# Optimization experiments

Hardware: AMD Instinct MI355X
Metric: run time of the kernel (lower is better)

## Reference

```python
import jax, jax.numpy as jnp
import numpy as np

EPS = 1e-5

def _dwconv1d(x, w):
    # x: [B,C,L], w: [C,k] depthwise kernel, same padding, no bias
    k = w.shape[1]
    return jax.lax.conv_general_dilated(
        x, w[:, None, :], window_strides=(1,), padding=[(k // 2, k // 2)],
        dimension_numbers=('NCH', 'OIH', 'NCH'), feature_group_count=x.shape[1])

def _bn1d(x, gamma, beta, mean, var):
    # eval-mode BatchNorm over channel dim of [B,C,L]
    scale = gamma / jnp.sqrt(var + EPS)
    return (x - mean[:, None]) * scale[:, None] + beta[:, None]

def _strip_pool(x, w3, w7, gamma, beta, mean, var):
    # mean of [identity, dwconv_k3, dwconv_k7] then BN
    out = (x + _dwconv1d(x, w3) + _dwconv1d(x, w7)) / 3.0
    return _bn1d(out, gamma, beta, mean, var)

def _hswish(x):
    return x * jnp.clip(x + 3.0, 0.0, 6.0) / 6.0

def setup_inputs() -> dict:
    key = jax.random.key(0)
    ks = jax.random.split(key, 8)
    B, C, H, W = 32, 256, 64, 64   # C = 2*inp
    MIP = 8                        # max(8, 128//32)
    O = 256                        # 2*oup
    f32 = jnp.float32
    x = jax.random.normal(ks[0], (B, C, H, W), f32)
    def bn_params(k, n):
        k1, k2 = jax.random.split(k)
        return (1.0 + 0.1 * jax.random.normal(k1, (n,), f32),      # gamma
                0.1 * jax.random.normal(k2, (n,), f32),            # beta
                jnp.zeros((n,), f32),                              # running_mean
                jnp.ones((n,), f32))                               # running_var
    sph_g, sph_b, sph_m, sph_v = bn_params(ks[1], C)
    spw_g, spw_b, spw_m, spw_v = bn_params(ks[2], C)
    bn1_g, bn1_b, bn1_m, bn1_v = bn_params(ks[3], MIP)
    s = 0.1
    return {
        'x': x,
        'sph_w3': s * jax.random.normal(ks[4], (C, 3), f32),
        'sph_w7': s * jax.random.normal(ks[4], (C, 7), f32),
        'sph_gamma': sph_g, 'sph_beta': sph_b, 'sph_mean': sph_m, 'sph_var': sph_v,
        'spw_w3': s * jax.random.normal(ks[5], (C, 3), f32),
        'spw_w7': s * jax.random.normal(ks[5], (C, 7), f32),
        'spw_gamma': spw_g, 'spw_beta': spw_b, 'spw_mean': spw_m, 'spw_var': spw_v,
        'conv1_w': s * jax.random.normal(ks[6], (MIP, C), f32),
        'bn1_gamma': bn1_g, 'bn1_beta': bn1_b, 'bn1_mean': bn1_m, 'bn1_var': bn1_v,
        'convh_w': s * jax.random.normal(ks[7], (O, MIP), f32),
        'convw_w': s * jax.random.normal(ks[7], (O, MIP), f32),
    }

def reference(x, sph_w3, sph_w7, sph_gamma, sph_beta, sph_mean, sph_var,
              spw_w3, spw_w7, spw_gamma, spw_beta, spw_mean, spw_var,
              conv1_w, bn1_gamma, bn1_beta, bn1_mean, bn1_var,
              convh_w, convw_w):
    B, C, H, W = x.shape
    # coordinate pooling -> strips [B,C,H] and [B,C,W]
    x_h = jnp.mean(x, axis=3)
    x_w = jnp.mean(x, axis=2)
    # multi-scale strip pooling
    x_h = _strip_pool(x_h, sph_w3, sph_w7, sph_gamma, sph_beta, sph_mean, sph_var)
    x_w = _strip_pool(x_w, spw_w3, spw_w7, spw_gamma, spw_beta, spw_mean, spw_var)
    # shared 1x1 conv + BN + h_swish on concatenated strip [B,C,H+W]
    y = jnp.concatenate([x_h, x_w], axis=2)
    y = jnp.einsum('mc,bcl->bml', conv1_w, y)
    y = _bn1d(y, bn1_gamma, bn1_beta, bn1_mean, bn1_var)
    y = _hswish(y)
    y_h, y_w = y[:, :, :H], y[:, :, H:]
    # per-direction gates [B,O,H] / [B,O,W]
    a_h = jax.nn.sigmoid(jnp.einsum('om,bmh->boh', convh_w, y_h))
    a_w = jax.nn.sigmoid(jnp.einsum('om,bmw->bow', convw_w, y_w))
    return x * a_h[:, :, :, None] * a_w[:, :, None, :]
```

## Files before the change

kernel.cpp:

```cpp
#include <hip/hip_runtime.h>
#include <math.h>

#define EPSF 1e-5f

__global__ __launch_bounds__(256) void k1_pool_strip(
    const float* __restrict__ x,
    const float* __restrict__ sph_w3, const float* __restrict__ sph_w7,
    const float* __restrict__ sph_g,  const float* __restrict__ sph_b,
    const float* __restrict__ sph_m,  const float* __restrict__ sph_v,
    const float* __restrict__ spw_w3, const float* __restrict__ spw_w7,
    const float* __restrict__ spw_g,  const float* __restrict__ spw_b,
    const float* __restrict__ spw_m,  const float* __restrict__ spw_v,
    float* __restrict__ sp)
{
    __shared__ __align__(16) float tile[64][68];
    __shared__ float mh[64];
    __shared__ float mw[64];

    const int plane = blockIdx.x;
    const int c = plane & 255;
    const float* xp = x + (size_t)plane * 4096;
    const int t = threadIdx.x;
    const int r = t >> 2, q = t & 3;

    const float4* src = (const float4*)(xp + r * 64 + q * 16);
    float4* dst = (float4*)&tile[r][q * 16];
    dst[0] = src[0]; dst[1] = src[1]; dst[2] = src[2]; dst[3] = src[3];
    __syncthreads();

    if (t < 64) {
        float s = 0.f;
        for (int rr = 0; rr < 64; ++rr) s += tile[rr][t];
        mw[t] = s * (1.f / 64.f);
    } else if (t < 128) {
        const int rr = t - 64;
        float s = 0.f;
        for (int i = 0; i < 64; ++i) s += tile[rr][(rr + i) & 63];
        mh[rr] = s * (1.f / 64.f);
    }
    __syncthreads();

    if (t < 128) {
        const int l = t & 63;
        const bool is_h = (t < 64);
        const float* m  = is_h ? mh     : mw;
        const float* w3 = is_h ? sph_w3 : spw_w3;
        const float* w7 = is_h ? sph_w7 : spw_w7;
        const float* g  = is_h ? sph_g  : spw_g;
        const float* bb = is_h ? sph_b  : spw_b;
        const float* mu = is_h ? sph_m  : spw_m;
        const float* vv = is_h ? sph_v  : spw_v;

        float v[7];
        #pragma unroll
        for (int j = 0; j < 7; ++j) {
            int idx = l - 3 + j;
            v[j] = (idx >= 0 && idx < 64) ? m[idx] : 0.f;
        }
        float c3 = w3[c*3+0]*v[2] + w3[c*3+1]*v[3] + w3[c*3+2]*v[4];
        float c7 = 0.f;
        #pragma unroll
        for (int j = 0; j < 7; ++j) c7 += w7[c*7+j]*v[j];

        float o = (v[3] + c3 + c7) * (1.f / 3.f);
        float scale = g[c] * rsqrtf(vv[c] + EPSF);
        o = (o - mu[c]) * scale + bb[c];
        sp[(size_t)plane * 128 + (is_h ? l : 64 + l)] = o;
    }
}

__global__ __launch_bounds__(256) void k2_mid(
    const float* __restrict__ sp,
    const float* __restrict__ conv1_w,
    const float* __restrict__ bn1_g, const float* __restrict__ bn1_b,
    const float* __restrict__ bn1_m, const float* __restrict__ bn1_v,
    const float* __restrict__ convh_w, const float* __restrict__ convw_w,
    float* __restrict__ a_h, float* __restrict__ a_w)
{
    __shared__ float w1[2048];
    __shared__ float wh[2048];
    __shared__ float ww[2048];
    __shared__ float y[8][128];
    __shared__ float bnp[4][8];

    const int b = blockIdx.x;
    const int t = threadIdx.x;

    for (int i = t; i < 2048; i += 256) {
        w1[i] = conv1_w[i];
        wh[i] = convh_w[i];
        ww[i] = convw_w[i];
    }
    if (t < 8) {
        bnp[0][t] = bn1_g[t]; bnp[1][t] = bn1_b[t];
        bnp[2][t] = bn1_m[t]; bnp[3][t] = bn1_v[t];
    }
    __syncthreads();

    const int l = t & 127, mb = t >> 7;
    const float* spb = sp + (size_t)b * 256 * 128;
    float acc[4] = {0.f, 0.f, 0.f, 0.f};
    for (int cc = 0; cc < 256; ++cc) {
        float vv = spb[cc * 128 + l];
        acc[0] += w1[(mb + 0) * 256 + cc] * vv;
        acc[1] += w1[(mb + 2) * 256 + cc] * vv;
        acc[2] += w1[(mb + 4) * 256 + cc] * vv;
        acc[3] += w1[(mb + 6) * 256 + cc] * vv;
    }
    #pragma unroll
    for (int j = 0; j < 4; ++j) {
        int m = mb + 2 * j;
        float val = acc[j];
        float scale = bnp[0][m] * rsqrtf(bnp[3][m] + EPSF);
        val = (val - bnp[2][m]) * scale + bnp[1][m];
        val = val * fminf(fmaxf(val + 3.f, 0.f), 6.f) * (1.f / 6.f);
        y[m][l] = val;
    }
    __syncthreads();

    float* ahb = a_h + (size_t)b * 256 * 64;
    float* awb = a_w + (size_t)b * 256 * 64;
    for (int i = 0; i < 64; ++i) {
        int idx = i * 256 + t;
        int o = idx >> 6, h = idx & 63;
        float sh = 0.f, sw = 0.f;
        #pragma unroll
        for (int m = 0; m < 8; ++m) {
            sh += wh[o * 8 + m] * y[m][h];
            sw += ww[o * 8 + m] * y[m][64 + h];
        }
        ahb[idx] = 1.f / (1.f + __expf(-sh));
        awb[idx] = 1.f / (1.f + __expf(-sw));
    }
}

__global__ __launch_bounds__(256) void k3_apply(
    const float* __restrict__ x,
    const float* __restrict__ a_h, const float* __restrict__ a_w,
    float* __restrict__ out)
{
    const size_t g = (size_t)blockIdx.x * 256 + threadIdx.x;
    float4 xv = ((const float4*)x)[g];
    const size_t idx = g * 4;
    const int w0 = (int)(idx & 63);
    const int h  = (int)((idx >> 6) & 63);
    const size_t bc = idx >> 12;
    const float ah = a_h[bc * 64 + h];
    const float4 aw = *(const float4*)(a_w + bc * 64 + w0);
    float4 o;
    o.x = xv.x * ah * aw.x;
    o.y = xv.y * ah * aw.y;
    o.z = xv.z * ah * aw.z;
    o.w = xv.w * ah * aw.w;
    ((float4*)out)[g] = o;
}

extern "C" void kernel_launch(void* const* d_in, const int* in_sizes, int n_in,
                              void* d_out, int out_size, void* d_ws, size_t ws_size,
                              hipStream_t stream) {
    const float* x       = (const float*)d_in[0];
    const float* sph_w3  = (const float*)d_in[1];
    const float* sph_w7  = (const float*)d_in[2];
    const float* sph_g   = (const float*)d_in[3];
    const float* sph_b   = (const float*)d_in[4];
    const float* sph_m   = (const float*)d_in[5];
    const float* sph_v   = (const float*)d_in[6];
    const float* spw_w3  = (const float*)d_in[7];
    const float* spw_w7  = (const float*)d_in[8];
    const float* spw_g   = (const float*)d_in[9];
    const float* spw_b   = (const float*)d_in[10];
    const float* spw_m   = (const float*)d_in[11];
    const float* spw_v   = (const float*)d_in[12];
    const float* conv1_w = (const float*)d_in[13];
    const float* bn1_g   = (const float*)d_in[14];
    const float* bn1_b   = (const float*)d_in[15];
    const float* bn1_m   = (const float*)d_in[16];
    const float* bn1_v   = (const float*)d_in[17];
    const float* convh_w = (const float*)d_in[18];
    const float* convw_w = (const float*)d_in[19];

    float* ws  = (float*)d_ws;
    float* sp  = ws;
    float* a_h = ws + 1048576;
    float* a_w = ws + 1048576 + 524288;

    const int B = 32, C = 256;

    k1_pool_strip<<<B * C, 256, 0, stream>>>(
        x, sph_w3, sph_w7, sph_g, sph_b, sph_m, sph_v,
        spw_w3, spw_w7, spw_g, spw_b, spw_m, spw_v, sp);

    k2_mid<<<B, 256, 0, stream>>>(
        sp, conv1_w, bn1_g, bn1_b, bn1_m, bn1_v, convh_w, convw_w, a_h, a_w);

    k3_apply<<<32768, 256, 0, stream>>>(x, a_h, a_w, (float*)d_out);
}
```

Measured before the change: 306.2 us.

## Parallelize strip reductions in pooling kernel and split mid kernel across strip chunks

In the pooling kernel, row sums are now computed in registers straight from the loaded float4 values, and column sums are split across all 256 threads as partial sums. Previously one or two warps did the serial 64-step reductions. The mid kernel now launches 8 blocks per batch instead of 1, each handling a 16-position chunk of the concatenated strip, which raises the block count from 32 to 256. The cost is extra shared-memory staging, and each block reloads the weights and its slice of the strip data.

```diff
diff --git a/kernel.cpp b/kernel.cpp
--- a/kernel.cpp
+++ b/kernel.cpp
@@ -14,6 +14,8 @@
     float* __restrict__ sp)
 {
     __shared__ __align__(16) float tile[64][68];
+    __shared__ __align__(16) float rpart[256];
+    __shared__ float cpart[4][64];
     __shared__ float mh[64];
     __shared__ float mw[64];
 
@@ -24,19 +26,26 @@
     const int r = t >> 2, q = t & 3;
 
     const float4* src = (const float4*)(xp + r * 64 + q * 16);
+    float4 v0 = src[0], v1 = src[1], v2 = src[2], v3 = src[3];
     float4* dst = (float4*)&tile[r][q * 16];
-    dst[0] = src[0]; dst[1] = src[1]; dst[2] = src[2]; dst[3] = src[3];
+    dst[0] = v0; dst[1] = v1; dst[2] = v2; dst[3] = v3;
+    rpart[t] = (v0.x + v0.y + v0.z + v0.w) + (v1.x + v1.y + v1.z + v1.w)
+             + (v2.x + v2.y + v2.z + v2.w) + (v3.x + v3.y + v3.z + v3.w);
+    __syncthreads();
+
+    {
+        const int cc = t & 63, qw = t >> 6;
+        float s = 0.f;
+        #pragma unroll
+        for (int i = 0; i < 16; ++i) s += tile[qw * 16 + i][cc];
+        cpart[qw][cc] = s;
+    }
     __syncthreads();
 
     if (t < 64) {
-        float s = 0.f;
-        for (int rr = 0; rr < 64; ++rr) s += tile[rr][t];
-        mw[t] = s * (1.f / 64.f);
-    } else if (t < 128) {
-        const int rr = t - 64;
-        float s = 0.f;
-        for (int i = 0; i < 64; ++i) s += tile[rr][(rr + i) & 63];
-        mh[rr] = s * (1.f / 64.f);
+        float4 rp = ((const float4*)rpart)[t];
+        mh[t] = (rp.x + rp.y + rp.z + rp.w) * (1.f / 64.f);
+        mw[t] = (cpart[0][t] + cpart[1][t] + cpart[2][t] + cpart[3][t]) * (1.f / 64.f);
     }
     __syncthreads();
 
@@ -77,60 +86,54 @@
     const float* __restrict__ convh_w, const float* __restrict__ convw_w,
     float* __restrict__ a_h, float* __restrict__ a_w)
 {
-    __shared__ float w1[2048];
-    __shared__ float wh[2048];
-    __shared__ float ww[2048];
-    __shared__ float y[8][128];
-    __shared__ float bnp[4][8];
-
-    const int b = blockIdx.x;
+    __shared__ float spc[256 * 16];
+    __shared__ float w1t[256 * 8];
+    __shared__ float wos[256 * 8];
+    __shared__ float ys[8 * 16];
+
+    const int b  = blockIdx.x >> 3;
+    const int lc = blockIdx.x & 7;
+    const int l0 = lc * 16;
+    const bool is_h = (l0 < 64);
     const int t = threadIdx.x;
 
-    for (int i = t; i < 2048; i += 256) {
-        w1[i] = conv1_w[i];
-        wh[i] = convh_w[i];
-        ww[i] = convw_w[i];
-    }
-    if (t < 8) {
-        bnp[0][t] = bn1_g[t]; bnp[1][t] = bn1_b[t];
-        bnp[2][t] = bn1_m[t]; bnp[3][t] = bn1_v[t];
-    }
-    __syncthreads();
-
-    const int l = t & 127, mb = t >> 7;
     const float* spb = sp + (size_t)b * 256 * 128;
-    float acc[4] = {0.f, 0.f, 0.f, 0.f};
-    for (int cc = 0; cc < 256; ++cc) {
-        float vv = spb[cc * 128 + l];
-        acc[0] += w1[(mb + 0) * 256 + cc] * vv;
-        acc[1] += w1[(mb + 2) * 256 + cc] * vv;
-        acc[2] += w1[(mb + 4) * 256 + cc] * vv;
-        acc[3] += w1[(mb + 6) * 256 + cc] * vv;
-    }
+    const float* wo  = is_h ? convh_w : convw_w;
+
+    for (int j = t; j < 4096; j += 256) {
+        int cc = j >> 4, li = j & 15;
+        spc[j] = spb[cc * 128 + l0 + li];
+    }
+    for (int j = t; j < 2048; j += 256) {
+        int cc = j >> 3, m = j & 7;
+        w1t[j] = conv1_w[m * 256 + cc];
+        wos[j] = wo[j];
+    }
+    __syncthreads();
+
+    if (t < 128) {
+        const int m = t >> 4, li = t & 15;
+        float acc = 0.f;
+        for (int cc = 0; cc < 256; ++cc)
+            acc += w1t[cc * 8 + m] * spc[cc * 16 + li];
+        float scale = bn1_g[m] * rsqrtf(bn1_v[m] + EPSF);
+        float val = (acc - bn1_m[m]) * scale + bn1_b[m];
+        val = val * fminf(fmaxf(val + 3.f, 0.f), 6.f) * (1.f / 6.f);
+        ys[m * 16 + li] = val;
+    }
+    __syncthreads();
+
+    float* ab = (is_h ? a_h : a_w) + (size_t)b * 256 * 64;
+    const int pos0 = is_h ? l0 : l0 - 64;
+    const int li = t & 15, ob = t >> 4;
     #pragma unroll
-    for (int j = 0; j < 4; ++j) {
-        int m = mb + 2 * j;
-        float val = acc[j];
-        float scale = bnp[0][m] * rsqrtf(bnp[3][m] + EPSF);
-        val = (val - bnp[2][m]) * scale + bnp[1][m];
-        val = val * fminf(fmaxf(val + 3.f, 0.f), 6.f) * (1.f / 6.f);
-        y[m][l] = val;
-    }
-    __syncthreads();
-
-    float* ahb = a_h + (size_t)b * 256 * 64;
-    float* awb = a_w + (size_t)b * 256 * 64;
-    for (int i = 0; i < 64; ++i) {
-        int idx = i * 256 + t;
-        int o = idx >> 6, h = idx & 63;
-        float sh = 0.f, sw = 0.f;
-        #pragma unroll
-        for (int m = 0; m < 8; ++m) {
-            sh += wh[o * 8 + m] * y[m][h];
-            sw += ww[o * 8 + m] * y[m][64 + h];
-        }
-        ahb[idx] = 1.f / (1.f + __expf(-sh));
-        awb[idx] = 1.f / (1.f + __expf(-sw));
+    for (int i = 0; i < 16; ++i) {
+        const int o = i * 16 + ob;
+        float s = 0.f;
+        #pragma unroll
+        for (int m = 0; m < 8; ++m)
+            s += wos[o * 8 + m] * ys[m * 16 + li];
+        ab[o * 64 + pos0 + li] = 1.f / (1.f + __expf(-s));
     }
 }
 
@@ -190,7 +193,7 @@
         x, sph_w3, sph_w7, sph_g, sph_b, sph_m, sph_v,
         spw_w3, spw_w7, spw_g, spw_b, spw_m, spw_v, sp);
 
-    k2_mid<<<B, 256, 0, stream>>>(
+    k2_mid<<<B * 8, 256, 0, stream>>>(
         sp, conv1_w, bn1_g, bn1_b, bn1_m, bn1_v, convh_w, convw_w, a_h, a_w);
 
     k3_apply<<<32768, 256, 0, stream>>>(x, a_h, a_w, (float*)d_out);
```

Result: faster. 292.0 us (-4.6%).
